# Kernel tuning notes

Measured on AMD Instinct MI355X. Metric: run time of the kernel, lower is better.

The kernel has to match this reference:

```python
import jax, jax.numpy as jnp
import numpy as np

EMBED_DIM = 512
NUM_HEADS = 8
HEAD_DIM = EMBED_DIM // NUM_HEADS
N = 4096
E = 131072
EPS = 1e-5
NEG = -1e9


def layer_norm(x, g, b):
    mu = jnp.mean(x, axis=-1, keepdims=True)
    var = jnp.mean(jnp.square(x - mu), axis=-1, keepdims=True)
    return (x - mu) * jax.lax.rsqrt(var + EPS) * g + b


def setup_inputs() -> dict:
    key = jax.random.key(0)
    ks = jax.random.split(key, 12)
    D = EMBED_DIM
    s = 1.0 / np.sqrt(D)
    return {
        "x": jax.random.normal(ks[0], (N, D), jnp.float32),
        "edge_index": jax.random.randint(ks[1], (2, E), 0, N, jnp.int64),
        "edge_weight": jax.random.uniform(ks[2], (E,), jnp.float32),
        "Wqkv": jax.random.normal(ks[3], (3 * D, D), jnp.float32) * s,
        "bqkv": jnp.zeros((3 * D,), jnp.float32),
        "Wo": jax.random.normal(ks[4], (D, D), jnp.float32) * s,
        "bo": jnp.zeros((D,), jnp.float32),
        "W1": jax.random.normal(ks[5], (D, D), jnp.float32) * s,
        "b1": jnp.zeros((D,), jnp.float32),
        "g1": jnp.ones((D,), jnp.float32),
        "beta1": jnp.zeros((D,), jnp.float32),
        "g2": jnp.ones((D,), jnp.float32),
        "beta2": jnp.zeros((D,), jnp.float32),
    }


def reference(x, edge_index, edge_weight, Wqkv, bqkv, Wo, bo, W1, b1, g1, beta1, g2, beta2):
    n = x.shape[0]
    # dense NxN additive bias: -1e9 everywhere, 0 on diagonal, edge weights at (dst, src)
    src, dst = edge_index[0], edge_index[1]
    diag = jnp.arange(n)
    bias = jnp.full((n, n), NEG, dtype=x.dtype)
    bias = bias.at[diag, diag].set(0.0)
    bias = bias.at[dst, src].set(edge_weight.astype(x.dtype))

    # multi-head self-attention (torch nn.MultiheadAttention semantics)
    qkv = x @ Wqkv.T + bqkv                       # (N, 3D)
    q, k, v = jnp.split(qkv, 3, axis=-1)          # each (N, D)
    q = q.reshape(n, NUM_HEADS, HEAD_DIM).transpose(1, 0, 2)  # (H, N, hd)
    k = k.reshape(n, NUM_HEADS, HEAD_DIM).transpose(1, 0, 2)
    v = v.reshape(n, NUM_HEADS, HEAD_DIM).transpose(1, 0, 2)
    scores = jnp.einsum("hnd,hmd->hnm", q, k) / np.sqrt(HEAD_DIM)  # (H, N, N)
    scores = scores + bias[None, :, :]
    attn = jax.nn.softmax(scores, axis=-1)
    out = jnp.einsum("hnm,hmd->hnd", attn, v)     # (H, N, hd)
    out = out.transpose(1, 0, 2).reshape(n, EMBED_DIM)
    attn_out = out @ Wo.T + bo

    # residual + LN + FFN (single linear, no activation) + residual + LN
    h = layer_norm(x + attn_out, g1, beta1)
    h = layer_norm(h + (h @ W1.T + b1), g2, beta2)
    return h
```

## Files before the change

kernel.cpp:

```cpp
#include <hip/hip_runtime.h>

#define NNODES 4096
#define DIM 512
#define QKVD 1536
#define MAXE 96

typedef __bf16 bf16_t;
typedef bf16_t bf16x8 __attribute__((ext_vector_type(8)));
typedef bf16_t bf16x2 __attribute__((ext_vector_type(2)));
typedef float f32x4 __attribute__((ext_vector_type(4)));
typedef unsigned int uint;

__global__ __launch_bounds__(256) void cast_all_k(const float* __restrict__ x,
                                                  const float* __restrict__ wqkv,
                                                  const float* __restrict__ wo,
                                                  const float* __restrict__ w1,
                                                  bf16_t* __restrict__ xb,
                                                  bf16_t* __restrict__ wqkvb,
                                                  bf16_t* __restrict__ wob,
                                                  bf16_t* __restrict__ w1b,
                                                  uint* __restrict__ deg) {
  int i = blockIdx.x * 256 + threadIdx.x;
  if (blockIdx.x < 16) deg[i] = 0u;
  const float* src;
  bf16_t* dst;
  int off;
  if (i < 524288) { src = x; dst = xb; off = i; }
  else if (i < 720896) { src = wqkv; dst = wqkvb; off = i - 524288; }
  else if (i < 786432) { src = wo; dst = wob; off = i - 720896; }
  else { src = w1; dst = w1b; off = i - 786432; }
  float4 v = ((const float4*)src)[off];
  dst[4 * off + 0] = (bf16_t)v.x;
  dst[4 * off + 1] = (bf16_t)v.y;
  dst[4 * off + 2] = (bf16_t)v.z;
  dst[4 * off + 3] = (bf16_t)v.w;
}

__global__ __launch_bounds__(256) void fill_bucket_k(const int* __restrict__ ei,
                                                     uint* __restrict__ deg,
                                                     int* __restrict__ colv,
                                                     uint* __restrict__ eidv, int E) {
  int e = blockIdx.x * 256 + threadIdx.x;
  if (e < E) {
    int src = ei[e] & (NNODES - 1);
    int dst = ei[E + e] & (NNODES - 1);
    uint pos = atomicAdd(&deg[dst], 1u);
    if (pos < MAXE) {
      colv[dst * MAXE + pos] = src;
      eidv[dst * MAXE + pos] = (uint)e + 1u;
    }
  }
}

template <bool OUT_BF16>
__global__ __launch_bounds__(256) void gemm_bt(const bf16_t* __restrict__ A,
                                               const bf16_t* __restrict__ B,
                                               const float* __restrict__ bias,
                                               void* __restrict__ Cout,
                                               int M, int Nt, int K) {
  __shared__ bf16_t As[128][40];
  __shared__ bf16_t Bs[64][40];
  const int t = threadIdx.x;
  const int lane = t & 63, w = t >> 6;
  const int wr = (w >> 1) * 64, wc = (w & 1) * 32;
  const int m0 = blockIdx.y * 128, n0 = blockIdx.x * 64;
  f32x4 acc[4][2] = {};
  const int r_ld = t >> 2;
  const int c_ld = (t & 3) * 8;

  for (int k0 = 0; k0 < K; k0 += 32) {
    *(int4*)&As[r_ld][c_ld] = *(const int4*)(A + (long)(m0 + r_ld) * K + k0 + c_ld);
    *(int4*)&As[r_ld + 64][c_ld] = *(const int4*)(A + (long)(m0 + r_ld + 64) * K + k0 + c_ld);
    *(int4*)&Bs[r_ld][c_ld] = *(const int4*)(B + (long)(n0 + r_ld) * K + k0 + c_ld);
    __syncthreads();
    bf16x8 af[4], bfr[2];
    const int kg = (lane >> 4) * 8;
#pragma unroll
    for (int i = 0; i < 4; ++i)
      af[i] = *(const bf16x8*)&As[wr + i * 16 + (lane & 15)][kg];
#pragma unroll
    for (int j = 0; j < 2; ++j)
      bfr[j] = *(const bf16x8*)&Bs[wc + j * 16 + (lane & 15)][kg];
#pragma unroll
    for (int i = 0; i < 4; ++i)
#pragma unroll
      for (int j = 0; j < 2; ++j)
        acc[i][j] = __builtin_amdgcn_mfma_f32_16x16x32_bf16(af[i], bfr[j], acc[i][j], 0, 0, 0);
    __syncthreads();
  }

  const int cr = (lane >> 4) * 4;
  const int cc = lane & 15;
#pragma unroll
  for (int i = 0; i < 4; ++i) {
#pragma unroll
    for (int j = 0; j < 2; ++j) {
      int n = n0 + wc + j * 16 + cc;
      float bv = bias[n];
#pragma unroll
      for (int r = 0; r < 4; ++r) {
        int m = m0 + wr + i * 16 + cr + r;
        float vv = acc[i][j][r] + bv;
        if (OUT_BF16)
          ((bf16_t*)Cout)[(long)m * Nt + n] = (bf16_t)vv;
        else
          ((float*)Cout)[(long)m * Nt + n] = vv;
      }
    }
  }
}

__global__ __launch_bounds__(512) void attn_fused_k(const bf16_t* __restrict__ qkv,
                                                    const float* __restrict__ ew,
                                                    const uint* __restrict__ deg,
                                                    const int* __restrict__ colv,
                                                    const uint* __restrict__ eidv,
                                                    bf16_t* __restrict__ outb) {
  __shared__ float scs[8][MAXE + 1];
  __shared__ int srcs[MAXE + 1];
  __shared__ uint eids[MAXE + 1];
  __shared__ int vld[MAXE + 1];
  __shared__ float invs_s[8];
  __shared__ float vacc[8][DIM];

  const int i = blockIdx.x;
  const int t = threadIdx.x;
  const int lane = t & 63, w = t >> 6;

  uint dg = deg[i];
  int L = (dg < (uint)MAXE) ? (int)dg : MAXE;
  int n = L + 1;

  if (t < L) {
    srcs[t] = colv[i * MAXE + t];
    eids[t] = eidv[i * MAXE + t];
  }
  if (t == L) { srcs[L] = i; eids[L] = 0u; }
  __syncthreads();

  if (t < n) {
    int sj = srcs[t];
    uint my = eids[t];
    int ok = 1;
    for (int j = 0; j < n; ++j)
      ok &= !((srcs[j] == sj) & (eids[j] > my));
    vld[t] = ok;
  }
  __syncthreads();

  const bf16x8 qv = *(const bf16x8*)(qkv + (long)i * QKVD + lane * 8);
  for (int e = w; e < n; e += 32) {
    int ec[4], val[4];
#pragma unroll
    for (int u = 0; u < 4; ++u) {
      int ee = e + u * 8;
      val[u] = ee < n;
      ec[u] = val[u] ? ee : e;
    }
    bf16x8 kr[4];
#pragma unroll
    for (int u = 0; u < 4; ++u)
      kr[u] = *(const bf16x8*)(qkv + (long)srcs[ec[u]] * QKVD + DIM + lane * 8);
    float d[4] = {0.f, 0.f, 0.f, 0.f};
#pragma unroll
    for (int j = 0; j < 8; ++j) {
      float q = (float)qv[j];
#pragma unroll
      for (int u = 0; u < 4; ++u) d[u] += q * (float)kr[u][j];
    }
#pragma unroll
    for (int o = 1; o < 8; o <<= 1) {
#pragma unroll
      for (int u = 0; u < 4; ++u) d[u] += __shfl_xor(d[u], o);
    }
    if ((lane & 7) == 0) {
      int h = lane >> 3;
#pragma unroll
      for (int u = 0; u < 4; ++u) {
        if (val[u]) {
          uint id = eids[ec[u]];
          float b = (id == 0u) ? 0.f : ew[id - 1u];
          scs[h][ec[u]] = vld[ec[u]] ? (d[u] * 0.125f + b) : -1e30f;
        }
      }
    }
  }
  __syncthreads();

  {
    float m = -1e30f;
    for (int e = lane; e < n; e += 64) m = fmaxf(m, scs[w][e]);
#pragma unroll
    for (int o = 32; o > 0; o >>= 1) m = fmaxf(m, __shfl_xor(m, o));
    float ps = 0.f;
    for (int e = lane; e < n; e += 64) {
      float ev = __expf(scs[w][e] - m);
      scs[w][e] = ev;
      ps += ev;
    }
#pragma unroll
    for (int o = 32; o > 0; o >>= 1) ps += __shfl_xor(ps, o);
    if (lane == 0) invs_s[w] = 1.f / ps;
  }
  __syncthreads();

  const int hl = lane >> 3;
  float a8[8] = {0.f, 0.f, 0.f, 0.f, 0.f, 0.f, 0.f, 0.f};
  for (int e = w; e < n; e += 32) {
    int ec[4];
    float p[4];
#pragma unroll
    for (int u = 0; u < 4; ++u) {
      int ee = e + u * 8;
      int vu = ee < n;
      ec[u] = vu ? ee : e;
      p[u] = vu ? scs[hl][ec[u]] : 0.f;
    }
    bf16x8 vr[4];
#pragma unroll
    for (int u = 0; u < 4; ++u)
      vr[u] = *(const bf16x8*)(qkv + (long)srcs[ec[u]] * QKVD + 2 * DIM + lane * 8);
#pragma unroll
    for (int j = 0; j < 8; ++j) {
#pragma unroll
      for (int u = 0; u < 4; ++u) a8[j] += p[u] * (float)vr[u][j];
    }
  }
#pragma unroll
  for (int j = 0; j < 8; ++j) vacc[w][lane * 8 + j] = a8[j];
  __syncthreads();

  {
    float s = 0.f;
#pragma unroll
    for (int ww = 0; ww < 8; ++ww) s += vacc[ww][t];
    outb[(long)i * DIM + t] = (bf16_t)(s * invs_s[t >> 6]);
  }
}

__global__ __launch_bounds__(64) void ln_k(const float* __restrict__ a,
                                           const float* __restrict__ b,
                                           const float* __restrict__ g,
                                           const float* __restrict__ beta,
                                           float* __restrict__ of,
                                           bf16_t* __restrict__ ob) {
  const int row = blockIdx.x;
  const int l = threadIdx.x;
  const float* pa = a + (long)row * DIM;
  const float* pb = b + (long)row * DIM;
  float v[8];
  float s = 0.f;
#pragma unroll
  for (int j = 0; j < 8; ++j) {
    int d = l + j * 64;
    v[j] = pa[d] + pb[d];
    s += v[j];
  }
#pragma unroll
  for (int o = 32; o > 0; o >>= 1) s += __shfl_xor(s, o);
  float mu = s * (1.f / 512.f);
  float q = 0.f;
#pragma unroll
  for (int j = 0; j < 8; ++j) {
    float dd = v[j] - mu;
    q += dd * dd;
  }
#pragma unroll
  for (int o = 32; o > 0; o >>= 1) q += __shfl_xor(q, o);
  float inv = rsqrtf(q * (1.f / 512.f) + 1e-5f);
#pragma unroll
  for (int j = 0; j < 8; ++j) {
    int d = l + j * 64;
    float y = (v[j] - mu) * inv * g[d] + beta[d];
    of[(long)row * DIM + d] = y;
    if (ob) ob[(long)row * DIM + d] = (bf16_t)y;
  }
}

extern "C" void kernel_launch(void* const* d_in, const int* in_sizes, int n_in,
                              void* d_out, int out_size, void* d_ws, size_t ws_size,
                              hipStream_t stream) {
  const float* x = (const float*)d_in[0];
  const int* ei = (const int*)d_in[1];
  const float* ew = (const float*)d_in[2];
  const float* Wqkv = (const float*)d_in[3];
  const float* bqkv = (const float*)d_in[4];
  const float* Wo = (const float*)d_in[5];
  const float* bo = (const float*)d_in[6];
  const float* W1 = (const float*)d_in[7];
  const float* b1 = (const float*)d_in[8];
  const float* g1 = (const float*)d_in[9];
  const float* be1 = (const float*)d_in[10];
  const float* g2 = (const float*)d_in[11];
  const float* be2 = (const float*)d_in[12];
  float* out = (float*)d_out;
  const int E = in_sizes[1] / 2;

  char* ws = (char*)d_ws;
  bf16_t* qkvb = (bf16_t*)(ws + 0);
  bf16_t* xb = (bf16_t*)(ws + 12582912);
  bf16_t* Wqkvb = (bf16_t*)(ws + 16777216);
  bf16_t* Wob = (bf16_t*)(ws + 18350080);
  bf16_t* W1b = (bf16_t*)(ws + 18874368);
  bf16_t* outb = (bf16_t*)(ws + 19398656);
  float* h = (float*)(ws + 23592960);
  bf16_t* hb = (bf16_t*)(ws + 31981568);
  float* f = (float*)(ws + 36175872);
  uint* deg = (uint*)(ws + 23592960);
  int* colv = (int*)(ws + 23609344);
  uint* eidv = (uint*)(ws + 25182208);
  float* attn_out = (float*)(ws + 0);

  cast_all_k<<<3328, 256, 0, stream>>>(x, Wqkv, Wo, W1, xb, Wqkvb, Wob, W1b, deg);
  fill_bucket_k<<<(E + 255) / 256, 256, 0, stream>>>(ei, deg, colv, eidv, E);

  gemm_bt<true><<<dim3(QKVD / 64, NNODES / 128), 256, 0, stream>>>(
      xb, Wqkvb, bqkv, (void*)qkvb, NNODES, QKVD, DIM);

  attn_fused_k<<<NNODES, 512, 0, stream>>>(qkvb, ew, deg, colv, eidv, outb);

  gemm_bt<false><<<dim3(DIM / 64, NNODES / 128), 256, 0, stream>>>(
      outb, Wob, bo, (void*)attn_out, NNODES, DIM, DIM);

  ln_k<<<NNODES, 64, 0, stream>>>(x, attn_out, g1, be1, h, hb);

  gemm_bt<false><<<dim3(DIM / 64, NNODES / 128), 256, 0, stream>>>(
      hb, W1b, b1, (void*)f, NNODES, DIM, DIM);

  ln_k<<<NNODES, 64, 0, stream>>>(h, f, g2, be2, out, nullptr);
}
```

Measured before the change: 119.4 us.

## Store K/V head-major and split sparse attention across head-group blocks

The QKV GEMM epilogue now writes K and V in a head-major layout (H, N, 64), with Q kept row-major. The attention kernel is split into 4 head groups per node (grid 4096x4), 256 threads each. Each wave handles 2 heads, with 32 lanes per head and bf16x2 loads per lane. The aim is to shrink each gathered K/V row to 128 bytes per head and to raise block-level parallelism. In exchange, the per-node edge dedup and bucket loads are repeated 4 times, the wave reductions get longer (5 shuffle steps), and the loads are narrower.

```diff
diff --git a/kernel.cpp b/kernel.cpp
--- a/kernel.cpp
+++ b/kernel.cpp
@@ -52,7 +52,7 @@
   }
 }
 
-template <bool OUT_BF16>
+template <int MODE>
 __global__ __launch_bounds__(256) void gemm_bt(const bf16_t* __restrict__ A,
                                                const bf16_t* __restrict__ B,
                                                const float* __restrict__ bias,
@@ -101,31 +101,47 @@
       for (int r = 0; r < 4; ++r) {
         int m = m0 + wr + i * 16 + cr + r;
         float vv = acc[i][j][r] + bv;
-        if (OUT_BF16)
+        if (MODE == 0) {
+          ((float*)Cout)[(long)m * Nt + n] = vv;
+        } else if (MODE == 1) {
           ((bf16_t*)Cout)[(long)m * Nt + n] = (bf16_t)vv;
-        else
-          ((float*)Cout)[(long)m * Nt + n] = vv;
+        } else {
+          bf16_t* C = (bf16_t*)Cout;
+          if (n < 512) {
+            C[(long)m * 512 + n] = (bf16_t)vv;
+          } else {
+            int reg = (n >= 1024);
+            int h = (n - 512 - reg * 512) >> 6;
+            int d = n & 63;
+            C[2097152 + (long)reg * 2097152 + h * 262144 + (long)m * 64 + d] = (bf16_t)vv;
+          }
+        }
       }
     }
   }
 }
 
-__global__ __launch_bounds__(512) void attn_fused_k(const bf16_t* __restrict__ qkv,
-                                                    const float* __restrict__ ew,
-                                                    const uint* __restrict__ deg,
-                                                    const int* __restrict__ colv,
-                                                    const uint* __restrict__ eidv,
-                                                    bf16_t* __restrict__ outb) {
-  __shared__ float scs[8][MAXE + 1];
+__global__ __launch_bounds__(256) void attn_hg_k(const bf16_t* __restrict__ qb,
+                                                 const bf16_t* __restrict__ kh,
+                                                 const bf16_t* __restrict__ vh,
+                                                 const float* __restrict__ ew,
+                                                 const uint* __restrict__ deg,
+                                                 const int* __restrict__ colv,
+                                                 const uint* __restrict__ eidv,
+                                                 bf16_t* __restrict__ outb) {
+  __shared__ float scs[2][MAXE + 1];
   __shared__ int srcs[MAXE + 1];
   __shared__ uint eids[MAXE + 1];
   __shared__ int vld[MAXE + 1];
-  __shared__ float invs_s[8];
-  __shared__ float vacc[8][DIM];
+  __shared__ float invs_s[2];
+  __shared__ float vacc[4][128];
 
   const int i = blockIdx.x;
+  const int hg = blockIdx.y;
   const int t = threadIdx.x;
   const int lane = t & 63, w = t >> 6;
+  const int hl = lane >> 5;
+  const int dl = (lane & 31) * 2;
 
   uint dg = deg[i];
   int L = (dg < (uint)MAXE) ? (int)dg : MAXE;
@@ -148,46 +164,49 @@
   }
   __syncthreads();
 
-  const bf16x8 qv = *(const bf16x8*)(qkv + (long)i * QKVD + lane * 8);
-  for (int e = w; e < n; e += 32) {
+  const int h = hg * 2 + hl;
+  const long hb = (long)h * (NNODES * 64);
+  float q0, q1;
+  {
+    bf16x2 qv = *(const bf16x2*)(qb + (long)i * 512 + h * 64 + dl);
+    q0 = (float)qv[0];
+    q1 = (float)qv[1];
+  }
+
+  for (int e = w; e < n; e += 16) {
     int ec[4], val[4];
 #pragma unroll
     for (int u = 0; u < 4; ++u) {
-      int ee = e + u * 8;
+      int ee = e + u * 4;
       val[u] = ee < n;
       ec[u] = val[u] ? ee : e;
     }
-    bf16x8 kr[4];
+    bf16x2 kr[4];
 #pragma unroll
     for (int u = 0; u < 4; ++u)
-      kr[u] = *(const bf16x8*)(qkv + (long)srcs[ec[u]] * QKVD + DIM + lane * 8);
-    float d[4] = {0.f, 0.f, 0.f, 0.f};
-#pragma unroll
-    for (int j = 0; j < 8; ++j) {
-      float q = (float)qv[j];
-#pragma unroll
-      for (int u = 0; u < 4; ++u) d[u] += q * (float)kr[u][j];
-    }
-#pragma unroll
-    for (int o = 1; o < 8; o <<= 1) {
+      kr[u] = *(const bf16x2*)(kh + hb + (long)srcs[ec[u]] * 64 + dl);
+    float d[4];
+#pragma unroll
+    for (int u = 0; u < 4; ++u) d[u] = q0 * (float)kr[u][0] + q1 * (float)kr[u][1];
+#pragma unroll
+    for (int o = 1; o < 32; o <<= 1) {
 #pragma unroll
       for (int u = 0; u < 4; ++u) d[u] += __shfl_xor(d[u], o);
     }
-    if ((lane & 7) == 0) {
-      int h = lane >> 3;
+    if ((lane & 31) == 0) {
 #pragma unroll
       for (int u = 0; u < 4; ++u) {
         if (val[u]) {
           uint id = eids[ec[u]];
           float b = (id == 0u) ? 0.f : ew[id - 1u];
-          scs[h][ec[u]] = vld[ec[u]] ? (d[u] * 0.125f + b) : -1e30f;
+          scs[hl][ec[u]] = vld[ec[u]] ? (d[u] * 0.125f + b) : -1e30f;
         }
       }
     }
   }
   __syncthreads();
 
-  {
+  if (w < 2) {
     float m = -1e30f;
     for (int e = lane; e < n; e += 64) m = fmaxf(m, scs[w][e]);
 #pragma unroll
@@ -204,37 +223,40 @@
   }
   __syncthreads();
 
-  const int hl = lane >> 3;
-  float a8[8] = {0.f, 0.f, 0.f, 0.f, 0.f, 0.f, 0.f, 0.f};
-  for (int e = w; e < n; e += 32) {
+  float a0 = 0.f, a1 = 0.f;
+  for (int e = w; e < n; e += 16) {
     int ec[4];
     float p[4];
 #pragma unroll
     for (int u = 0; u < 4; ++u) {
-      int ee = e + u * 8;
+      int ee = e + u * 4;
       int vu = ee < n;
       ec[u] = vu ? ee : e;
       p[u] = vu ? scs[hl][ec[u]] : 0.f;
     }
-    bf16x8 vr[4];
+    bf16x2 vr[4];
 #pragma unroll
     for (int u = 0; u < 4; ++u)
-      vr[u] = *(const bf16x8*)(qkv + (long)srcs[ec[u]] * QKVD + 2 * DIM + lane * 8);
-#pragma unroll
-    for (int j = 0; j < 8; ++j) {
-#pragma unroll
-      for (int u = 0; u < 4; ++u) a8[j] += p[u] * (float)vr[u][j];
-    }
-  }
-#pragma unroll
-  for (int j = 0; j < 8; ++j) vacc[w][lane * 8 + j] = a8[j];
-  __syncthreads();
-
-  {
-    float s = 0.f;
-#pragma unroll
-    for (int ww = 0; ww < 8; ++ww) s += vacc[ww][t];
-    outb[(long)i * DIM + t] = (bf16_t)(s * invs_s[t >> 6]);
+      vr[u] = *(const bf16x2*)(vh + hb + (long)srcs[ec[u]] * 64 + dl);
+#pragma unroll
+    for (int u = 0; u < 4; ++u) {
+      a0 += p[u] * (float)vr[u][0];
+      a1 += p[u] * (float)vr[u][1];
+    }
+  }
+  vacc[w][hl * 64 + dl] = a0;
+  vacc[w][hl * 64 + dl + 1] = a1;
+  __syncthreads();
+
+  if (t < 64) {
+    int d0 = 2 * t;
+    float inv = invs_s[d0 >> 6];
+    float s0 = vacc[0][d0] + vacc[1][d0] + vacc[2][d0] + vacc[3][d0];
+    float s1 = vacc[0][d0 + 1] + vacc[1][d0 + 1] + vacc[2][d0 + 1] + vacc[3][d0 + 1];
+    bf16x2 o2;
+    o2[0] = (bf16_t)(s0 * inv);
+    o2[1] = (bf16_t)(s1 * inv);
+    *(bf16x2*)(outb + (long)i * 512 + hg * 128 + d0) = o2;
   }
 }
 
@@ -297,7 +319,10 @@
   const int E = in_sizes[1] / 2;
 
   char* ws = (char*)d_ws;
-  bf16_t* qkvb = (bf16_t*)(ws + 0);
+  bf16_t* qsplit = (bf16_t*)(ws + 0);
+  bf16_t* qb = qsplit;
+  bf16_t* khp = qsplit + 2097152;
+  bf16_t* vhp = qsplit + 4194304;
   bf16_t* xb = (bf16_t*)(ws + 12582912);
   bf16_t* Wqkvb = (bf16_t*)(ws + 16777216);
   bf16_t* Wob = (bf16_t*)(ws + 18350080);
@@ -314,17 +339,17 @@
   cast_all_k<<<3328, 256, 0, stream>>>(x, Wqkv, Wo, W1, xb, Wqkvb, Wob, W1b, deg);
   fill_bucket_k<<<(E + 255) / 256, 256, 0, stream>>>(ei, deg, colv, eidv, E);
 
-  gemm_bt<true><<<dim3(QKVD / 64, NNODES / 128), 256, 0, stream>>>(
-      xb, Wqkvb, bqkv, (void*)qkvb, NNODES, QKVD, DIM);
-
-  attn_fused_k<<<NNODES, 512, 0, stream>>>(qkvb, ew, deg, colv, eidv, outb);
-
-  gemm_bt<false><<<dim3(DIM / 64, NNODES / 128), 256, 0, stream>>>(
+  gemm_bt<2><<<dim3(QKVD / 64, NNODES / 128), 256, 0, stream>>>(
+      xb, Wqkvb, bqkv, (void*)qsplit, NNODES, QKVD, DIM);
+
+  attn_hg_k<<<dim3(NNODES, 4), 256, 0, stream>>>(qb, khp, vhp, ew, deg, colv, eidv, outb);
+
+  gemm_bt<0><<<dim3(DIM / 64, NNODES / 128), 256, 0, stream>>>(
       outb, Wob, bo, (void*)attn_out, NNODES, DIM, DIM);
 
   ln_k<<<NNODES, 64, 0, stream>>>(x, attn_out, g1, be1, h, hb);
 
-  gemm_bt<false><<<dim3(DIM / 64, NNODES / 128), 256, 0, stream>>>(
+  gemm_bt<0><<<dim3(DIM / 64, NNODES / 128), 256, 0, stream>>>(
       hb, W1b, b1, (void*)f, NNODES, DIM, DIM);
 
   ln_k<<<NNODES, 64, 0, stream>>>(h, f, g2, be2, out, nullptr);
```

Result: slower. 157.6 us (+32.1%).

## Prefetch first 64 neighbor K/V rows and edge biases before dedup pass

Applied to the files above, without the earlier changes.

The sparse attention kernel now issues loads for the first 8 K and V rows per wave, plus their edge-weight biases, right after the neighbor list is staged and before the duplicate-edge validity scan and barrier. The global-load latency is meant to overlap the O(n^2) dedup loop and the softmax phase, instead of being paid twice in the score and value loops. Neighbors beyond 64 fall back to the per-edge loop without unrolling. This adds about 128 VGPRs of prefetched bf16x8 data per thread, which may reduce occupancy, and the tail loop loses the previous 4-way load batching.

```diff
diff --git a/kernel.cpp b/kernel.cpp
--- a/kernel.cpp
+++ b/kernel.cpp
@@ -138,6 +138,28 @@
   if (t == L) { srcs[L] = i; eids[L] = 0u; }
   __syncthreads();
 
+  const bf16x8 qv = *(const bf16x8*)(qkv + (long)i * QKVD + lane * 8);
+  int val[8], ec[8];
+#pragma unroll
+  for (int u = 0; u < 8; ++u) {
+    int ee = w + 8 * u;
+    val[u] = ee < n;
+    ec[u] = val[u] ? ee : 0;
+  }
+  bf16x8 kpre[8], vpre[8];
+#pragma unroll
+  for (int u = 0; u < 8; ++u) {
+    long rb = (long)srcs[ec[u]] * QKVD;
+    kpre[u] = *(const bf16x8*)(qkv + rb + DIM + lane * 8);
+    vpre[u] = *(const bf16x8*)(qkv + rb + 2 * DIM + lane * 8);
+  }
+  float bpre[8];
+#pragma unroll
+  for (int u = 0; u < 8; ++u) {
+    uint id = eids[ec[u]];
+    bpre[u] = (id == 0u) ? 0.f : ew[id - 1u];
+  }
+
   if (t < n) {
     int sj = srcs[t];
     uint my = eids[t];
@@ -148,41 +170,29 @@
   }
   __syncthreads();
 
-  const bf16x8 qv = *(const bf16x8*)(qkv + (long)i * QKVD + lane * 8);
-  for (int e = w; e < n; e += 32) {
-    int ec[4], val[4];
-#pragma unroll
-    for (int u = 0; u < 4; ++u) {
-      int ee = e + u * 8;
-      val[u] = ee < n;
-      ec[u] = val[u] ? ee : e;
-    }
-    bf16x8 kr[4];
-#pragma unroll
-    for (int u = 0; u < 4; ++u)
-      kr[u] = *(const bf16x8*)(qkv + (long)srcs[ec[u]] * QKVD + DIM + lane * 8);
-    float d[4] = {0.f, 0.f, 0.f, 0.f};
-#pragma unroll
-    for (int j = 0; j < 8; ++j) {
-      float q = (float)qv[j];
-#pragma unroll
-      for (int u = 0; u < 4; ++u) d[u] += q * (float)kr[u][j];
-    }
-#pragma unroll
-    for (int o = 1; o < 8; o <<= 1) {
-#pragma unroll
-      for (int u = 0; u < 4; ++u) d[u] += __shfl_xor(d[u], o);
-    }
+#pragma unroll
+  for (int u = 0; u < 8; ++u) {
+    float d = 0.f;
+#pragma unroll
+    for (int j = 0; j < 8; ++j) d += (float)qv[j] * (float)kpre[u][j];
+#pragma unroll
+    for (int o = 1; o < 8; o <<= 1) d += __shfl_xor(d, o);
+    if (((lane & 7) == 0) & val[u]) {
+      int e = w + 8 * u;
+      scs[lane >> 3][e] = vld[e] ? (d * 0.125f + bpre[u]) : -1e30f;
+    }
+  }
+  for (int e = w + 64; e < n; e += 8) {
+    const bf16x8 ka = *(const bf16x8*)(qkv + (long)srcs[e] * QKVD + DIM + lane * 8);
+    float d = 0.f;
+#pragma unroll
+    for (int j = 0; j < 8; ++j) d += (float)qv[j] * (float)ka[j];
+#pragma unroll
+    for (int o = 1; o < 8; o <<= 1) d += __shfl_xor(d, o);
     if ((lane & 7) == 0) {
-      int h = lane >> 3;
-#pragma unroll
-      for (int u = 0; u < 4; ++u) {
-        if (val[u]) {
-          uint id = eids[ec[u]];
-          float b = (id == 0u) ? 0.f : ew[id - 1u];
-          scs[h][ec[u]] = vld[ec[u]] ? (d[u] * 0.125f + b) : -1e30f;
-        }
-      }
+      uint id = eids[e];
+      float b = (id == 0u) ? 0.f : ew[id - 1u];
+      scs[lane >> 3][e] = vld[e] ? (d * 0.125f + b) : -1e30f;
     }
   }
   __syncthreads();
@@ -206,25 +216,17 @@
 
   const int hl = lane >> 3;
   float a8[8] = {0.f, 0.f, 0.f, 0.f, 0.f, 0.f, 0.f, 0.f};
-  for (int e = w; e < n; e += 32) {
-    int ec[4];
-    float p[4];
-#pragma unroll
-    for (int u = 0; u < 4; ++u) {
-      int ee = e + u * 8;
-      int vu = ee < n;
-      ec[u] = vu ? ee : e;
-      p[u] = vu ? scs[hl][ec[u]] : 0.f;
-    }
-    bf16x8 vr[4];
-#pragma unroll
-    for (int u = 0; u < 4; ++u)
-      vr[u] = *(const bf16x8*)(qkv + (long)srcs[ec[u]] * QKVD + 2 * DIM + lane * 8);
-#pragma unroll
-    for (int j = 0; j < 8; ++j) {
-#pragma unroll
-      for (int u = 0; u < 4; ++u) a8[j] += p[u] * (float)vr[u][j];
-    }
+#pragma unroll
+  for (int u = 0; u < 8; ++u) {
+    float p = val[u] ? scs[hl][w + 8 * u] : 0.f;
+#pragma unroll
+    for (int j = 0; j < 8; ++j) a8[j] += p * (float)vpre[u][j];
+  }
+  for (int e = w + 64; e < n; e += 8) {
+    const bf16x8 vv = *(const bf16x8*)(qkv + (long)srcs[e] * QKVD + 2 * DIM + lane * 8);
+    float p = scs[hl][e];
+#pragma unroll
+    for (int j = 0; j < 8; ++j) a8[j] += p * (float)vv[j];
   }
 #pragma unroll
   for (int j = 0; j < 8; ++j) vacc[w][lane * 8 + j] = a8[j];
```

Result: slower. 129.6 us (+8.6%).
